# Kernel optimization log

Hardware: AMD Instinct MI355X
Metric: run time of the kernel (lower is better)

## Reference

```python
import jax, jax.numpy as jnp
import numpy as np

OBJ_DIM, REL_DIM, EFF_DIM = 3, 1, 1
REL_HID, OBJ_HID = 150, 100
B, N, E = 4, 2048, 8192
N_RECUR = 1


def _linear_init(k, fan_in, fan_out):
    s = 1.0 / np.sqrt(fan_in)
    k1, k2 = jax.random.split(k)
    W = jax.random.uniform(k1, (fan_in, fan_out), jnp.float32, -s, s)
    b = jax.random.uniform(k2, (fan_out,), jnp.float32, -s, s)
    return W, b


def setup_inputs() -> dict:
    key = jax.random.key(0)
    ks = jax.random.split(key, 9)
    objects = jax.random.normal(ks[0], (B, N, OBJ_DIM), jnp.float32)
    # one-hot incidence matrices [B, N, E]: column e selects sender/receiver node of edge e
    snd_idx = jax.random.randint(ks[1], (B, E), 0, N)
    rcv_idx = jax.random.randint(ks[2], (B, E), 0, N)
    sender_relations = jax.nn.one_hot(snd_idx, N, dtype=jnp.float32).transpose(0, 2, 1)
    receiver_relations = jax.nn.one_hot(rcv_idx, N, dtype=jnp.float32).transpose(0, 2, 1)
    relation_info = jax.random.normal(ks[3], (B, REL_DIM, E), jnp.float32)
    rW1, rb1 = _linear_init(ks[4], 2 * OBJ_DIM + REL_DIM, REL_HID)
    rW2, rb2 = _linear_init(ks[5], REL_HID, REL_HID)
    rW3, rb3 = _linear_init(ks[6], REL_HID, EFF_DIM)
    oW1, ob1 = _linear_init(ks[7], OBJ_DIM + EFF_DIM, OBJ_HID)
    oW2, ob2 = _linear_init(ks[8], OBJ_HID, OBJ_DIM)
    return dict(objects=objects, sender_relations=sender_relations,
                receiver_relations=receiver_relations, relation_info=relation_info,
                rW1=rW1, rb1=rb1, rW2=rW2, rb2=rb2, rW3=rW3, rb3=rb3,
                oW1=oW1, ob1=ob1, oW2=oW2, ob2=ob2)


def _relational(x, rW1, rb1, rW2, rb2, rW3, rb3):
    # per-edge MLP: [B, E, 2*obj+rel] -> [B, E, eff], sigmoid head (edge weight)
    h = jax.nn.relu(x @ rW1 + rb1)
    h = jax.nn.relu(h @ rW2 + rb2)
    return jax.nn.sigmoid(h @ rW3 + rb3)


def _object(x, oW1, ob1, oW2, ob2):
    # per-node MLP: [B, N, obj+eff] -> [B, N, obj]
    h = jax.nn.relu(x @ oW1 + ob1)
    return h @ oW2 + ob2


def reference(objects, sender_relations, receiver_relations, relation_info,
              rW1, rb1, rW2, rb2, rW3, rb3, oW1, ob1, oW2, ob2):
    obj = objects                                   # [B, N, D]
    rel_t = relation_info.transpose(0, 2, 1)        # [B, E, REL_DIM]
    for _ in range(N_RECUR):
        # gather via dense one-hot matmul (faithful to torch.matmul(obj.t(), S))
        snd = jnp.einsum('bnd,bne->bed', obj, sender_relations)
        rcv = jnp.einsum('bnd,bne->bed', obj, receiver_relations)
        inter = jnp.concatenate([snd, rcv, rel_t], axis=-1)      # [B, E, 2D+rel]
        eff = _relational(inter, rW1, rb1, rW2, rb2, rW3, rb3)   # [B, E, eff]
        eff_rcv = jnp.einsum('bne,bef->bnf', receiver_relations, eff)  # scatter-add to nodes
        agg = jnp.concatenate([obj, eff_rcv], axis=-1)           # [B, N, D+eff]
        obj = _object(agg, oW1, ob1, oW2, ob2)
    snd = jnp.einsum('bnd,bne->bed', obj, sender_relations)
    rcv = jnp.einsum('bnd,bne->bed', obj, receiver_relations)
    inter = jnp.concatenate([snd, rcv, rel_t], axis=-1)
    edge_weights = _relational(inter, rW1, rb1, rW2, rb2, rW3, rb3)  # [B, E, eff]
    return edge_weights
```

## Files before the change

### kernel.cpp

```cpp
#include <hip/hip_runtime.h>

#define BB 4
#define NN 2048
#define EE 8192
#define RH 150
#define RHP 152
#define LSTR 156
#define OH 100
#define JPW 19

typedef float f4_t __attribute__((ext_vector_type(4)));

__global__ __launch_bounds__(256) void scan_prep_kernel(
    const float* __restrict__ S, const float* __restrict__ R,
    const float* __restrict__ rW2, const float* __restrict__ rb2,
    const float* __restrict__ rW3,
    int* __restrict__ snd_idx, int* __restrict__ rcv_idx,
    float* __restrict__ W2p, float* __restrict__ b2p, float* __restrict__ W3p,
    float* __restrict__ eff_rcv)
{
    const unsigned gtid = blockIdx.x * 256u + threadIdx.x;

    if (gtid < RHP * RHP) {
        const int k = (int)gtid / RHP, j = (int)gtid - k * RHP;
        W2p[gtid] = (k < RH && j < RH) ? rW2[k * RH + j] : 0.0f;
    }
    if (gtid < RHP) {
        b2p[gtid] = (gtid < RH) ? rb2[gtid] : 0.0f;
        W3p[gtid] = (gtid < RH) ? rW3[gtid] : 0.0f;
    }
    if (gtid < BB * NN) eff_rcv[gtid] = 0.0f;

    const bool second = blockIdx.x >= 2048;
    const float* __restrict__ M = second ? R : S;
    int* __restrict__ idx = second ? rcv_idx : snd_idx;

    const unsigned total4 = (unsigned)BB * NN * EE / 4u;
    unsigned i = (blockIdx.x & 2047u) * 256u + threadIdx.x;
    const unsigned stride = 2048u * 256u;
    for (; i < total4; i += stride) {
        const f4_t v = __builtin_nontemporal_load(reinterpret_cast<const f4_t*>(M) + i);
        if (v.x > 0.5f || v.y > 0.5f || v.z > 0.5f || v.w > 0.5f) {
            const unsigned flat = i * 4u;
            const unsigned e = flat & (EE - 1u);
            const unsigned n = (flat >> 13) & (NN - 1u);
            const unsigned b = flat >> 24;
            if (v.x > 0.5f) idx[b * EE + e + 0u] = (int)n;
            if (v.y > 0.5f) idx[b * EE + e + 1u] = (int)n;
            if (v.z > 0.5f) idx[b * EE + e + 2u] = (int)n;
            if (v.w > 0.5f) idx[b * EE + e + 3u] = (int)n;
        }
    }
}

__device__ __forceinline__ float edge_mlp_body(
    const float x[7], int t, int e, int jg,
    const float* __restrict__ W1, const float* __restrict__ b1,
    const float* __restrict__ W2p, const float* __restrict__ b2p,
    const float* __restrict__ W3p, const float* __restrict__ b3,
    float* __restrict__ h1s, float* __restrict__ red)
{
    for (int j = jg; j < LSTR; j += 8) {
        float v = 0.0f;
        if (j < RH) {
            v = b1[j];
#pragma unroll
            for (int k = 0; k < 7; ++k) v = fmaf(x[k], W1[k * RH + j], v);
            v = fmaxf(v, 0.0f);
        }
        h1s[e * LSTR + j] = v;
    }
    __syncthreads();

    const int w = __builtin_amdgcn_readfirstlane(jg);
    const int jbase = w * JPW;

    float acc[JPW];
#pragma unroll
    for (int m = 0; m < JPW; ++m) acc[m] = b2p[jbase + m];

    const float* hrow = h1s + e * LSTR;
    for (int kc = 0; kc < RHP; kc += 4) {
        const float4 hv = *reinterpret_cast<const float4*>(hrow + kc);
        const float* r0 = W2p + (kc + 0) * RHP + jbase;
        const float* r1 = r0 + RHP;
        const float* r2 = r1 + RHP;
        const float* r3 = r2 + RHP;
#pragma unroll
        for (int m = 0; m < JPW; ++m) {
            float a = acc[m];
            a = fmaf(hv.x, r0[m], a);
            a = fmaf(hv.y, r1[m], a);
            a = fmaf(hv.z, r2[m], a);
            a = fmaf(hv.w, r3[m], a);
            acc[m] = a;
        }
    }

    float o = 0.0f;
#pragma unroll
    for (int m = 0; m < JPW; ++m)
        o = fmaf(fmaxf(acc[m], 0.0f), W3p[jbase + m], o);

    red[t] = o;
    __syncthreads();

    float tot = b3[0];
#pragma unroll
    for (int i = 0; i < 8; ++i) tot += red[(t & 63) + 64 * i];
    return 1.0f / (1.0f + __expf(-tot));
}

__global__ __launch_bounds__(512) void edge0_kernel(
    const float* __restrict__ obj,
    const int* __restrict__ snd_idx, const int* __restrict__ rcv_idx,
    const float* __restrict__ rel,
    const float* __restrict__ W1, const float* __restrict__ b1,
    const float* __restrict__ W2p, const float* __restrict__ b2p,
    const float* __restrict__ W3p, const float* __restrict__ b3,
    float* __restrict__ eff_rcv)
{
    __shared__ float h1s[64 * LSTR];
    __shared__ float red[512];

    const int t = (int)threadIdx.x;
    const int ebase = (int)blockIdx.x * 64;
    const int e = t & 63;
    const int jg = t >> 6;
    const int eg = ebase + e;
    const int b = eg >> 13;

    float x[7];
    {
        const int sn = snd_idx[eg];
        const int rn = rcv_idx[eg];
        const float* ps = obj + ((b << 11) + sn) * 3;
        const float* pr = obj + ((b << 11) + rn) * 3;
        x[0] = ps[0]; x[1] = ps[1]; x[2] = ps[2];
        x[3] = pr[0]; x[4] = pr[1]; x[5] = pr[2];
        x[6] = rel[eg];
    }

    const float eff = edge_mlp_body(x, t, e, jg, W1, b1, W2p, b2p, W3p, b3, h1s, red);
    if (t < 64) atomicAdd(&eff_rcv[(b << 11) + rcv_idx[eg]], eff);
}

__global__ __launch_bounds__(512) void edge1_kernel(
    const float* __restrict__ objects, const float* __restrict__ eff_rcv,
    const int* __restrict__ snd_idx, const int* __restrict__ rcv_idx,
    const float* __restrict__ rel,
    const float* __restrict__ oW1, const float* __restrict__ ob1,
    const float* __restrict__ oW2, const float* __restrict__ ob2,
    const float* __restrict__ W1, const float* __restrict__ b1,
    const float* __restrict__ W2p, const float* __restrict__ b2p,
    const float* __restrict__ W3p, const float* __restrict__ b3,
    float* __restrict__ out)
{
    __shared__ float h1s[64 * LSTR];
    __shared__ float red[512];
    __shared__ int   nds[128];
    __shared__ float onew[128][3];

    const int t = (int)threadIdx.x;
    const int ebase = (int)blockIdx.x * 64;
    const int e = t & 63;
    const int jg = t >> 6;
    const int eg = ebase + e;
    const int b = ebase >> 13;

    if (t < 64)       nds[t] = snd_idx[ebase + t];
    else if (t < 128) nds[t] = rcv_idx[ebase + (t - 64)];
    __syncthreads();

    if (t < 128) {
        const int node = (b << 11) + nds[t];
        const float x0 = objects[node * 3 + 0];
        const float x1 = objects[node * 3 + 1];
        const float x2 = objects[node * 3 + 2];
        const float x3 = eff_rcv[node];
        float a0 = ob2[0], a1 = ob2[1], a2 = ob2[2];
#pragma unroll 4
        for (int j = 0; j < OH; ++j) {
            float h = ob1[j];
            h = fmaf(x0, oW1[0 * OH + j], h);
            h = fmaf(x1, oW1[1 * OH + j], h);
            h = fmaf(x2, oW1[2 * OH + j], h);
            h = fmaf(x3, oW1[3 * OH + j], h);
            h = fmaxf(h, 0.0f);
            a0 = fmaf(h, oW2[j * 3 + 0], a0);
            a1 = fmaf(h, oW2[j * 3 + 1], a1);
            a2 = fmaf(h, oW2[j * 3 + 2], a2);
        }
        onew[t][0] = a0; onew[t][1] = a1; onew[t][2] = a2;
    }
    __syncthreads();

    float x[7];
    x[0] = onew[e][0];      x[1] = onew[e][1];      x[2] = onew[e][2];
    x[3] = onew[64 + e][0]; x[4] = onew[64 + e][1]; x[5] = onew[64 + e][2];
    x[6] = rel[eg];

    const float eff = edge_mlp_body(x, t, e, jg, W1, b1, W2p, b2p, W3p, b3, h1s, red);
    if (t < 64) out[eg] = eff;
}

extern "C" void kernel_launch(void* const* d_in, const int* in_sizes, int n_in,
                              void* d_out, int out_size, void* d_ws, size_t ws_size,
                              hipStream_t stream) {
    (void)in_sizes; (void)n_in; (void)out_size; (void)ws_size;

    const float* objects = (const float*)d_in[0];
    const float* S       = (const float*)d_in[1];
    const float* R       = (const float*)d_in[2];
    const float* rel     = (const float*)d_in[3];
    const float* rW1     = (const float*)d_in[4];
    const float* rb1     = (const float*)d_in[5];
    const float* rW2     = (const float*)d_in[6];
    const float* rb2     = (const float*)d_in[7];
    const float* rW3     = (const float*)d_in[8];
    const float* rb3     = (const float*)d_in[9];
    const float* oW1     = (const float*)d_in[10];
    const float* ob1     = (const float*)d_in[11];
    const float* oW2     = (const float*)d_in[12];
    const float* ob2     = (const float*)d_in[13];

    char* ws = (char*)d_ws;
    int*   snd_idx = (int*)(ws + 0);
    int*   rcv_idx = (int*)(ws + (128 << 10));
    float* eff_rcv = (float*)(ws + (256 << 10));
    float* W2p     = (float*)(ws + (288 << 10));
    float* b2p     = (float*)(ws + (384 << 10));
    float* W3p     = (float*)(ws + (385 << 10));

    scan_prep_kernel<<<4096, 256, 0, stream>>>(
        S, R, rW2, rb2, rW3, snd_idx, rcv_idx, W2p, b2p, W3p, eff_rcv);

    edge0_kernel<<<(BB * EE) / 64, 512, 0, stream>>>(
        objects, snd_idx, rcv_idx, rel, rW1, rb1, W2p, b2p, W3p, rb3, eff_rcv);

    edge1_kernel<<<(BB * EE) / 64, 512, 0, stream>>>(
        objects, eff_rcv, snd_idx, rcv_idx, rel, oW1, ob1, oW2, ob2,
        rW1, rb1, W2p, b2p, W3p, rb3, (float*)d_out);
}
```

Measured before the change: 136.1 us.

## Use bf16 MFMA for the hidden edge-MLP layer with transposed padded weights

```diff
diff --git a/kernel.cpp b/kernel.cpp
--- a/kernel.cpp
+++ b/kernel.cpp
@@ -1,33 +1,41 @@
 #include <hip/hip_runtime.h>
+#include <hip/hip_bf16.h>
 
 #define BB 4
 #define NN 2048
 #define EE 8192
 #define RH 150
-#define RHP 152
-#define LSTR 156
+#define NP 160
+#define HSTR 168
+#define RSTR 36
 #define OH 100
-#define JPW 19
-
-typedef float f4_t __attribute__((ext_vector_type(4)));
+
+typedef float f4_t   __attribute__((ext_vector_type(4)));
+typedef short short8 __attribute__((ext_vector_type(8)));
+typedef float f32x4  __attribute__((ext_vector_type(4)));
+
+__device__ __forceinline__ unsigned short f2bf(float f) {
+    __hip_bfloat16 h = __float2bfloat16(f);
+    return *reinterpret_cast<unsigned short*>(&h);
+}
 
 __global__ __launch_bounds__(256) void scan_prep_kernel(
     const float* __restrict__ S, const float* __restrict__ R,
     const float* __restrict__ rW2, const float* __restrict__ rb2,
     const float* __restrict__ rW3,
     int* __restrict__ snd_idx, int* __restrict__ rcv_idx,
-    float* __restrict__ W2p, float* __restrict__ b2p, float* __restrict__ W3p,
-    float* __restrict__ eff_rcv)
+    unsigned short* __restrict__ w2t, float* __restrict__ b2p,
+    float* __restrict__ w3p, float* __restrict__ eff_rcv)
 {
     const unsigned gtid = blockIdx.x * 256u + threadIdx.x;
 
-    if (gtid < RHP * RHP) {
-        const int k = (int)gtid / RHP, j = (int)gtid - k * RHP;
-        W2p[gtid] = (k < RH && j < RH) ? rW2[k * RH + j] : 0.0f;
-    }
-    if (gtid < RHP) {
+    if (gtid < NP * NP) {
+        const int n = (int)gtid / NP, k = (int)gtid - n * NP;
+        w2t[gtid] = (n < RH && k < RH) ? f2bf(rW2[k * RH + n]) : (unsigned short)0;
+    }
+    if (gtid < NP) {
         b2p[gtid] = (gtid < RH) ? rb2[gtid] : 0.0f;
-        W3p[gtid] = (gtid < RH) ? rW3[gtid] : 0.0f;
+        w3p[gtid] = (gtid < RH) ? rW3[gtid] : 0.0f;
     }
     if (gtid < BB * NN) eff_rcv[gtid] = 0.0f;
 
@@ -54,13 +62,16 @@
 }
 
 __device__ __forceinline__ float edge_mlp_body(
-    const float x[7], int t, int e, int jg,
+    const float x[7], int t,
     const float* __restrict__ W1, const float* __restrict__ b1,
-    const float* __restrict__ W2p, const float* __restrict__ b2p,
-    const float* __restrict__ W3p, const float* __restrict__ b3,
-    float* __restrict__ h1s, float* __restrict__ red)
-{
-    for (int j = jg; j < LSTR; j += 8) {
+    const unsigned short* __restrict__ w2t, const float* __restrict__ b2p,
+    const float* __restrict__ w3p, const float* __restrict__ b3,
+    unsigned short* __restrict__ h1bf, float* __restrict__ red2)
+{
+    const int e  = t & 63;
+    const int w  = t >> 6;
+
+    for (int j = w; j < NP; j += 8) {
         float v = 0.0f;
         if (j < RH) {
             v = b1[j];
@@ -68,66 +79,77 @@
             for (int k = 0; k < 7; ++k) v = fmaf(x[k], W1[k * RH + j], v);
             v = fmaxf(v, 0.0f);
         }
-        h1s[e * LSTR + j] = v;
-    }
-    __syncthreads();
-
-    const int w = __builtin_amdgcn_readfirstlane(jg);
-    const int jbase = w * JPW;
-
-    float acc[JPW];
-#pragma unroll
-    for (int m = 0; m < JPW; ++m) acc[m] = b2p[jbase + m];
-
-    const float* hrow = h1s + e * LSTR;
-    for (int kc = 0; kc < RHP; kc += 4) {
-        const float4 hv = *reinterpret_cast<const float4*>(hrow + kc);
-        const float* r0 = W2p + (kc + 0) * RHP + jbase;
-        const float* r1 = r0 + RHP;
-        const float* r2 = r1 + RHP;
-        const float* r3 = r2 + RHP;
-#pragma unroll
-        for (int m = 0; m < JPW; ++m) {
-            float a = acc[m];
-            a = fmaf(hv.x, r0[m], a);
-            a = fmaf(hv.y, r1[m], a);
-            a = fmaf(hv.z, r2[m], a);
-            a = fmaf(hv.w, r3[m], a);
-            acc[m] = a;
-        }
-    }
-
-    float o = 0.0f;
-#pragma unroll
-    for (int m = 0; m < JPW; ++m)
-        o = fmaf(fmaxf(acc[m], 0.0f), W3p[jbase + m], o);
-
-    red[t] = o;
-    __syncthreads();
-
+        h1bf[e * HSTR + j] = f2bf(v);
+    }
+    __syncthreads();
+
+    const int lane = t & 63;
+    const int g = w >> 2;
+    const int m = w & 3;
+    const int c  = lane & 15;
+    const int kg = lane >> 4;
+
+    f32x4 acc[5];
+#pragma unroll
+    for (int nti = 0; nti < 5; ++nti) {
+        const float bi = b2p[(g * 5 + nti) * 16 + c];
+        acc[nti] = (f32x4){bi, bi, bi, bi};
+    }
+
+#pragma unroll
+    for (int ks = 0; ks < 5; ++ks) {
+        const short8 a = *reinterpret_cast<const short8*>(
+            &h1bf[(m * 16 + c) * HSTR + ks * 32 + kg * 8]);
+#pragma unroll
+        for (int nti = 0; nti < 5; ++nti) {
+            const int n = (g * 5 + nti) * 16 + c;
+            const short8 bfr = *reinterpret_cast<const short8*>(
+                &w2t[n * NP + ks * 32 + kg * 8]);
+            acc[nti] = __builtin_amdgcn_mfma_f32_16x16x32_bf16(a, bfr, acc[nti], 0, 0, 0);
+        }
+    }
+
+    float p0 = 0.0f, p1 = 0.0f, p2 = 0.0f, p3 = 0.0f;
+#pragma unroll
+    for (int nti = 0; nti < 5; ++nti) {
+        const int n = (g * 5 + nti) * 16 + c;
+        const float w3v = w3p[n];
+        p0 = fmaf(fmaxf(acc[nti][0], 0.0f), w3v, p0);
+        p1 = fmaf(fmaxf(acc[nti][1], 0.0f), w3v, p1);
+        p2 = fmaf(fmaxf(acc[nti][2], 0.0f), w3v, p2);
+        p3 = fmaf(fmaxf(acc[nti][3], 0.0f), w3v, p3);
+    }
+    {
+        const int er = m * 16 + kg * 4;
+        red2[(er + 0) * RSTR + g * 16 + c] = p0;
+        red2[(er + 1) * RSTR + g * 16 + c] = p1;
+        red2[(er + 2) * RSTR + g * 16 + c] = p2;
+        red2[(er + 3) * RSTR + g * 16 + c] = p3;
+    }
+    __syncthreads();
+
+    if (t >= 64) return 0.0f;
     float tot = b3[0];
 #pragma unroll
-    for (int i = 0; i < 8; ++i) tot += red[(t & 63) + 64 * i];
+    for (int i = 0; i < 32; ++i) tot += red2[t * RSTR + i];
     return 1.0f / (1.0f + __expf(-tot));
 }
 
-__global__ __launch_bounds__(512) void edge0_kernel(
+__global__ __launch_bounds__(512, 4) void edge0_kernel(
     const float* __restrict__ obj,
     const int* __restrict__ snd_idx, const int* __restrict__ rcv_idx,
     const float* __restrict__ rel,
     const float* __restrict__ W1, const float* __restrict__ b1,
-    const float* __restrict__ W2p, const float* __restrict__ b2p,
-    const float* __restrict__ W3p, const float* __restrict__ b3,
+    const unsigned short* __restrict__ w2t, const float* __restrict__ b2p,
+    const float* __restrict__ w3p, const float* __restrict__ b3,
     float* __restrict__ eff_rcv)
 {
-    __shared__ float h1s[64 * LSTR];
-    __shared__ float red[512];
+    __shared__ unsigned short h1bf[64 * HSTR];
+    __shared__ float red2[64 * RSTR];
 
     const int t = (int)threadIdx.x;
     const int ebase = (int)blockIdx.x * 64;
-    const int e = t & 63;
-    const int jg = t >> 6;
-    const int eg = ebase + e;
+    const int eg = ebase + (t & 63);
     const int b = eg >> 13;
 
     float x[7];
@@ -141,30 +163,29 @@
         x[6] = rel[eg];
     }
 
-    const float eff = edge_mlp_body(x, t, e, jg, W1, b1, W2p, b2p, W3p, b3, h1s, red);
+    const float eff = edge_mlp_body(x, t, W1, b1, w2t, b2p, w3p, b3, h1bf, red2);
     if (t < 64) atomicAdd(&eff_rcv[(b << 11) + rcv_idx[eg]], eff);
 }
 
-__global__ __launch_bounds__(512) void edge1_kernel(
+__global__ __launch_bounds__(512, 4) void edge1_kernel(
     const float* __restrict__ objects, const float* __restrict__ eff_rcv,
     const int* __restrict__ snd_idx, const int* __restrict__ rcv_idx,
     const float* __restrict__ rel,
     const float* __restrict__ oW1, const float* __restrict__ ob1,
     const float* __restrict__ oW2, const float* __restrict__ ob2,
     const float* __restrict__ W1, const float* __restrict__ b1,
-    const float* __restrict__ W2p, const float* __restrict__ b2p,
-    const float* __restrict__ W3p, const float* __restrict__ b3,
+    const unsigned short* __restrict__ w2t, const float* __restrict__ b2p,
+    const float* __restrict__ w3p, const float* __restrict__ b3,
     float* __restrict__ out)
 {
-    __shared__ float h1s[64 * LSTR];
-    __shared__ float red[512];
+    __shared__ unsigned short h1bf[64 * HSTR];
+    __shared__ float red2[64 * RSTR];
     __shared__ int   nds[128];
     __shared__ float onew[128][3];
 
     const int t = (int)threadIdx.x;
     const int ebase = (int)blockIdx.x * 64;
     const int e = t & 63;
-    const int jg = t >> 6;
     const int eg = ebase + e;
     const int b = ebase >> 13;
 
@@ -200,7 +221,7 @@
     x[3] = onew[64 + e][0]; x[4] = onew[64 + e][1]; x[5] = onew[64 + e][2];
     x[6] = rel[eg];
 
-    const float eff = edge_mlp_body(x, t, e, jg, W1, b1, W2p, b2p, W3p, b3, h1s, red);
+    const float eff = edge_mlp_body(x, t, W1, b1, w2t, b2p, w3p, b3, h1bf, red2);
     if (t < 64) out[eg] = eff;
 }
 
@@ -225,20 +246,20 @@
     const float* ob2     = (const float*)d_in[13];
 
     char* ws = (char*)d_ws;
-    int*   snd_idx = (int*)(ws + 0);
-    int*   rcv_idx = (int*)(ws + (128 << 10));
-    float* eff_rcv = (float*)(ws + (256 << 10));
-    float* W2p     = (float*)(ws + (288 << 10));
-    float* b2p     = (float*)(ws + (384 << 10));
-    float* W3p     = (float*)(ws + (385 << 10));
+    int*            snd_idx = (int*)(ws + 0);
+    int*            rcv_idx = (int*)(ws + (128 << 10));
+    float*          eff_rcv = (float*)(ws + (256 << 10));
+    unsigned short* w2t     = (unsigned short*)(ws + (288 << 10));
+    float*          b2p     = (float*)(ws + (344 << 10));
+    float*          w3p     = (float*)(ws + (345 << 10));
 
     scan_prep_kernel<<<4096, 256, 0, stream>>>(
-        S, R, rW2, rb2, rW3, snd_idx, rcv_idx, W2p, b2p, W3p, eff_rcv);
+        S, R, rW2, rb2, rW3, snd_idx, rcv_idx, w2t, b2p, w3p, eff_rcv);
 
     edge0_kernel<<<(BB * EE) / 64, 512, 0, stream>>>(
-        objects, snd_idx, rcv_idx, rel, rW1, rb1, W2p, b2p, W3p, rb3, eff_rcv);
+        objects, snd_idx, rcv_idx, rel, rW1, rb1, w2t, b2p, w3p, rb3, eff_rcv);
 
     edge1_kernel<<<(BB * EE) / 64, 512, 0, stream>>>(
         objects, eff_rcv, snd_idx, rcv_idx, rel, oW1, ob1, oW2, ob2,
-        rW1, rb1, W2p, b2p, W3p, rb3, (float*)d_out);
-}
+        rW1, rb1, w2t, b2p, w3p, rb3, (float*)d_out);
+}
```

Result: faster. 113.9 us (-16.3%).
